# Optimization experiments

Measured on AMD Instinct MI355X. Metric: run time of the kernel, lower is better.

The kernel has to match this reference:

```python
import jax, jax.numpy as jnp
import numpy as np

EPS = 1e-12  # F.normalize eps

def _l2_normalize(x):
    n = jnp.linalg.norm(x, axis=-1, keepdims=True)
    return x / jnp.maximum(n, EPS)

def setup_inputs() -> dict:
    key = jax.random.key(0)
    k1, k2 = jax.random.split(key)
    B, C, F = 32768, 1000, 256
    features = jax.random.normal(k1, (B, F), dtype=jnp.float32)
    prototypes = jax.random.normal(k2, (C, F), dtype=jnp.float32)
    distance_scale = jnp.ones((1,), dtype=jnp.float32)
    temperature = jnp.ones((1,), dtype=jnp.float32)
    return {"features": features, "prototypes": prototypes,
            "distance_scale": distance_scale, "temperature": temperature}

def reference(features, prototypes, distance_scale, temperature):
    # Normalize both sides to the unit sphere (F.normalize, p=2, eps=1e-12)
    fn = _l2_normalize(features)       # [B, F]
    pn = _l2_normalize(prototypes)     # [C, F]
    # For unit vectors: ||a-b||_2 / sqrt(2) = sqrt(1 - a.b)
    cos = jnp.einsum('bf,cf->bc', fn, pn)          # [B, C]
    dist = jnp.sqrt(jnp.maximum(1.0 - cos, 0.0))   # cdist(...)/sqrt(2)
    iso = jnp.abs(distance_scale[0]) * dist
    logits = -(iso + jnp.mean(iso, axis=1, keepdims=True))
    return logits / temperature[0]
```

## Files before the change

### kernel.cpp

```cpp
#include <hip/hip_runtime.h>


typedef __attribute__((ext_vector_type(8))) short short8;
typedef __attribute__((ext_vector_type(4))) float f32x4;
typedef __fp16 h2 __attribute__((ext_vector_type(2)));

union U16 { uint4 u4; short8 s8; };

static __device__ __forceinline__ unsigned short f2bf(float x){
  union { float f; unsigned u; } v; v.f = x;
  unsigned r = v.u + 0x7fffu + ((v.u >> 16) & 1u);
  return (unsigned short)(r >> 16);
}

#define CPAD 1024

__global__ void norm_protos_kernel(const float* __restrict__ src,
                                   unsigned short* __restrict__ dst, int C)
{
  const int wave = threadIdx.x >> 6;
  const int lane = threadIdx.x & 63;
  const int row  = blockIdx.x * 4 + wave;
  const int t    = row >> 4;
  const int l16  = row & 15;
  const int s    = lane >> 3;
  const int quad = (lane >> 1) & 3;
  const int j    = (lane & 1) * 4;

  ushort4 o = {0, 0, 0, 0};
  if (row < C){
    const float4 v = *(const float4*)(src + row * 256 + lane * 4);
    float ss = v.x*v.x + v.y*v.y + v.z*v.z + v.w*v.w;
    #pragma unroll
    for (int off = 32; off; off >>= 1) ss += __shfl_xor(ss, off);
    const float inv = 1.0f / fmaxf(sqrtf(ss), 1e-12f);
    o.x = f2bf(v.x * inv); o.y = f2bf(v.y * inv);
    o.z = f2bf(v.z * inv); o.w = f2bf(v.w * inv);
  }
  *(ushort4*)(dst + ((size_t)((t*8 + s)*64 + quad*16 + l16))*8 + j) = o;
}

__global__ __launch_bounds__(256, 2)
void fused_kernel(const float* __restrict__ feats,
                  const unsigned short* __restrict__ pnw,
                  const float* __restrict__ ds,
                  const float* __restrict__ temp,
                  float* __restrict__ out, int C)
{
  __shared__ float wsum[2][16][4];

  const int tid  = threadIdx.x;
  const int wave = tid >> 6;
  const int lane = tid & 63;
  const int quad = lane >> 4;
  const int l16  = lane & 15;
  const long rowbase = (long)blockIdx.x * 32;

  short8 ffrag[2][8];
  #pragma unroll
  for (int rg = 0; rg < 2; ++rg){
    const float* rp = feats + (rowbase + rg*16 + l16) * 256 + quad*8;
    float4 va[8], vb[8];
    float ss = 0.f;
    #pragma unroll
    for (int s = 0; s < 8; ++s){
      va[s] = *(const float4*)(rp + s*32);
      vb[s] = *(const float4*)(rp + s*32 + 4);
      ss += va[s].x*va[s].x + va[s].y*va[s].y + va[s].z*va[s].z + va[s].w*va[s].w;
      ss += vb[s].x*vb[s].x + vb[s].y*vb[s].y + vb[s].z*vb[s].z + vb[s].w*vb[s].w;
    }
    ss += __shfl_xor(ss, 16);
    ss += __shfl_xor(ss, 32);
    const float inv = __builtin_amdgcn_rcpf(__builtin_amdgcn_sqrtf(fmaxf(ss, 1e-24f)));
    #pragma unroll
    for (int s = 0; s < 8; ++s){
      U16 u;
      u.u4.x = (unsigned)f2bf(va[s].x*inv) | ((unsigned)f2bf(va[s].y*inv) << 16);
      u.u4.y = (unsigned)f2bf(va[s].z*inv) | ((unsigned)f2bf(va[s].w*inv) << 16);
      u.u4.z = (unsigned)f2bf(vb[s].x*inv) | ((unsigned)f2bf(vb[s].y*inv) << 16);
      u.u4.w = (unsigned)f2bf(vb[s].z*inv) | ((unsigned)f2bf(vb[s].w*inv) << 16);
      ffrag[rg][s] = u.s8;
    }
  }

  const uint4* tp = (const uint4*)pnw + (size_t)(wave*16)*512 + lane;

  h2 dd0[16][2];
  h2 dd1[16][2];
  float rsum0 = 0.f, rsum1 = 0.f;

  #pragma unroll
  for (int wt = 0; wt < 16; ++wt){
    const uint4* bp = tp + (size_t)wt*512;
    short8 pfrag[8];
    #pragma unroll
    for (int s = 0; s < 8; ++s){ U16 u; u.u4 = bp[s*64]; pfrag[s] = u.s8; }

    f32x4 acc0 = (f32x4){0.f, 0.f, 0.f, 0.f};
    f32x4 acc1 = (f32x4){0.f, 0.f, 0.f, 0.f};
    #pragma unroll
    for (int s = 0; s < 8; ++s){
      acc0 = __builtin_amdgcn_mfma_f32_16x16x32_bf16(pfrag[s], ffrag[0][s], acc0, 0, 0, 0);
      acc1 = __builtin_amdgcn_mfma_f32_16x16x32_bf16(pfrag[s], ffrag[1][s], acc1, 0, 0, 0);
    }

    float a0 = __builtin_amdgcn_sqrtf(fmaxf(1.0f - acc0[0], 0.0f));
    float a1 = __builtin_amdgcn_sqrtf(fmaxf(1.0f - acc0[1], 0.0f));
    float a2 = __builtin_amdgcn_sqrtf(fmaxf(1.0f - acc0[2], 0.0f));
    float a3 = __builtin_amdgcn_sqrtf(fmaxf(1.0f - acc0[3], 0.0f));
    float b0 = __builtin_amdgcn_sqrtf(fmaxf(1.0f - acc1[0], 0.0f));
    float b1 = __builtin_amdgcn_sqrtf(fmaxf(1.0f - acc1[1], 0.0f));
    float b2 = __builtin_amdgcn_sqrtf(fmaxf(1.0f - acc1[2], 0.0f));
    float b3 = __builtin_amdgcn_sqrtf(fmaxf(1.0f - acc1[3], 0.0f));

    const int cls = wave*256 + wt*16 + quad*4;
    rsum0 += (cls < C) ? (a0 + a1 + a2 + a3) : 0.0f;
    rsum1 += (cls < C) ? (b0 + b1 + b2 + b3) : 0.0f;

    dd0[wt][0] = __builtin_amdgcn_cvt_pkrtz(a0, a1);
    dd0[wt][1] = __builtin_amdgcn_cvt_pkrtz(a2, a3);
    dd1[wt][0] = __builtin_amdgcn_cvt_pkrtz(b0, b1);
    dd1[wt][1] = __builtin_amdgcn_cvt_pkrtz(b2, b3);
  }

  rsum0 += __shfl_xor(rsum0, 16);
  rsum0 += __shfl_xor(rsum0, 32);
  rsum1 += __shfl_xor(rsum1, 16);
  rsum1 += __shfl_xor(rsum1, 32);
  if (quad == 0){
    wsum[0][l16][wave] = rsum0;
    wsum[1][l16][wave] = rsum1;
  }
  __syncthreads();

  const float nscale = -fabsf(ds[0]) / temp[0];
  const float4 w0 = *(const float4*)&wsum[0][l16][0];
  const float4 w1 = *(const float4*)&wsum[1][l16][0];
  const float bias0 = nscale * ((w0.x + w0.y + w0.z + w0.w) / (float)C);
  const float bias1 = nscale * ((w1.x + w1.y + w1.z + w1.w) / (float)C);

  float* orow0 = out + (rowbase + l16) * (size_t)C;
  float* orow1 = out + (rowbase + 16 + l16) * (size_t)C;
  #pragma unroll
  for (int wt = 0; wt < 16; ++wt){
    const int cls = wave*256 + wt*16 + quad*4;
    if (cls < C){
      float4 o0, o1;
      o0.x = fmaf(nscale, (float)dd0[wt][0][0], bias0);
      o0.y = fmaf(nscale, (float)dd0[wt][0][1], bias0);
      o0.z = fmaf(nscale, (float)dd0[wt][1][0], bias0);
      o0.w = fmaf(nscale, (float)dd0[wt][1][1], bias0);
      o1.x = fmaf(nscale, (float)dd1[wt][0][0], bias1);
      o1.y = fmaf(nscale, (float)dd1[wt][0][1], bias1);
      o1.z = fmaf(nscale, (float)dd1[wt][1][0], bias1);
      o1.w = fmaf(nscale, (float)dd1[wt][1][1], bias1);
      *(float4*)(orow0 + cls) = o0;
      *(float4*)(orow1 + cls) = o1;
    }
  }
}

extern "C" void kernel_launch(void* const* d_in, const int* in_sizes, int n_in,
                              void* d_out, int out_size, void* d_ws, size_t ws_size,
                              hipStream_t stream) {
  const float* features = (const float*)d_in[0];
  const float* protos   = (const float*)d_in[1];
  const float* dscale   = (const float*)d_in[2];
  const float* temp     = (const float*)d_in[3];
  float* out = (float*)d_out;

  const int F = 256;
  const int B = in_sizes[0] / F;
  const int C = in_sizes[1] / F;

  unsigned short* pnw = (unsigned short*)d_ws;

  norm_protos_kernel<<<CPAD/4, 256, 0, stream>>>(protos, pnw, C);
  fused_kernel<<<B/32, 256, 0, stream>>>(features, pnw, dscale, temp, out, C);
}
```

Baseline: 189.3 us.

## Prefetch prototype tiles two ahead and stage distances in LDS

Prototype fragments are loaded into a triple-buffered register ring, two tiles ahead of the MFMA loop, so global load latency overlaps with compute. Packed fp16 distances now go to a 64KB shared-memory buffer instead of 64 registers, which frees VGPRs for the prefetch buffers. The MFMA section is wrapped in s_setprio to favour matrix issue. The cost is 64KB of LDS per block, which may limit occupancy below the launch_bounds target of 2 blocks, plus extra LDS write and read traffic.

Result: faster. 185.2 us (-2.1%).

```diff
diff --git a/kernel.cpp b/kernel.cpp
--- a/kernel.cpp
+++ b/kernel.cpp
@@ -6,6 +6,7 @@
 typedef __fp16 h2 __attribute__((ext_vector_type(2)));
 
 union U16 { uint4 u4; short8 s8; };
+union H2U { h2 h; unsigned u; };
 
 static __device__ __forceinline__ unsigned short f2bf(float x){
   union { float f; unsigned u; } v; v.f = x;
@@ -47,6 +48,7 @@
                   const float* __restrict__ temp,
                   float* __restrict__ out, int C)
 {
+  __shared__ uint4 ddbuf[4 * 16 * 64];
   __shared__ float wsum[2][16][4];
 
   const int tid  = threadIdx.x;
@@ -85,24 +87,31 @@
 
   const uint4* tp = (const uint4*)pnw + (size_t)(wave*16)*512 + lane;
 
-  h2 dd0[16][2];
-  h2 dd1[16][2];
+  U16 buf[3][8];
+  #pragma unroll
+  for (int s = 0; s < 8; ++s) buf[0][s].u4 = tp[s*64];
+  #pragma unroll
+  for (int s = 0; s < 8; ++s) buf[1][s].u4 = tp[512 + s*64];
+
   float rsum0 = 0.f, rsum1 = 0.f;
 
   #pragma unroll
   for (int wt = 0; wt < 16; ++wt){
-    const uint4* bp = tp + (size_t)wt*512;
-    short8 pfrag[8];
-    #pragma unroll
-    for (int s = 0; s < 8; ++s){ U16 u; u.u4 = bp[s*64]; pfrag[s] = u.s8; }
+    if (wt + 2 < 16){
+      const uint4* np = tp + (size_t)(wt + 2)*512;
+      #pragma unroll
+      for (int s = 0; s < 8; ++s) buf[(wt + 2) % 3][s].u4 = np[s*64];
+    }
 
     f32x4 acc0 = (f32x4){0.f, 0.f, 0.f, 0.f};
     f32x4 acc1 = (f32x4){0.f, 0.f, 0.f, 0.f};
+    __builtin_amdgcn_s_setprio(1);
     #pragma unroll
     for (int s = 0; s < 8; ++s){
-      acc0 = __builtin_amdgcn_mfma_f32_16x16x32_bf16(pfrag[s], ffrag[0][s], acc0, 0, 0, 0);
-      acc1 = __builtin_amdgcn_mfma_f32_16x16x32_bf16(pfrag[s], ffrag[1][s], acc1, 0, 0, 0);
+      acc0 = __builtin_amdgcn_mfma_f32_16x16x32_bf16(buf[wt % 3][s].s8, ffrag[0][s], acc0, 0, 0, 0);
+      acc1 = __builtin_amdgcn_mfma_f32_16x16x32_bf16(buf[wt % 3][s].s8, ffrag[1][s], acc1, 0, 0, 0);
     }
+    __builtin_amdgcn_s_setprio(0);
 
     float a0 = __builtin_amdgcn_sqrtf(fmaxf(1.0f - acc0[0], 0.0f));
     float a1 = __builtin_amdgcn_sqrtf(fmaxf(1.0f - acc0[1], 0.0f));
@@ -117,10 +126,13 @@
     rsum0 += (cls < C) ? (a0 + a1 + a2 + a3) : 0.0f;
     rsum1 += (cls < C) ? (b0 + b1 + b2 + b3) : 0.0f;
 
-    dd0[wt][0] = __builtin_amdgcn_cvt_pkrtz(a0, a1);
-    dd0[wt][1] = __builtin_amdgcn_cvt_pkrtz(a2, a3);
-    dd1[wt][0] = __builtin_amdgcn_cvt_pkrtz(b0, b1);
-    dd1[wt][1] = __builtin_amdgcn_cvt_pkrtz(b2, b3);
+    H2U p0, p1, p2, p3;
+    p0.h = __builtin_amdgcn_cvt_pkrtz(a0, a1);
+    p1.h = __builtin_amdgcn_cvt_pkrtz(a2, a3);
+    p2.h = __builtin_amdgcn_cvt_pkrtz(b0, b1);
+    p3.h = __builtin_amdgcn_cvt_pkrtz(b2, b3);
+    uint4 pk; pk.x = p0.u; pk.y = p1.u; pk.z = p2.u; pk.w = p3.u;
+    ddbuf[(wave*16 + wt)*64 + lane] = pk;
   }
 
   rsum0 += __shfl_xor(rsum0, 16);
@@ -145,15 +157,18 @@
   for (int wt = 0; wt < 16; ++wt){
     const int cls = wave*256 + wt*16 + quad*4;
     if (cls < C){
+      const uint4 pk = ddbuf[(wave*16 + wt)*64 + lane];
+      H2U p0, p1, p2, p3;
+      p0.u = pk.x; p1.u = pk.y; p2.u = pk.z; p3.u = pk.w;
       float4 o0, o1;
-      o0.x = fmaf(nscale, (float)dd0[wt][0][0], bias0);
-      o0.y = fmaf(nscale, (float)dd0[wt][0][1], bias0);
-      o0.z = fmaf(nscale, (float)dd0[wt][1][0], bias0);
-      o0.w = fmaf(nscale, (float)dd0[wt][1][1], bias0);
-      o1.x = fmaf(nscale, (float)dd1[wt][0][0], bias1);
-      o1.y = fmaf(nscale, (float)dd1[wt][0][1], bias1);
-      o1.z = fmaf(nscale, (float)dd1[wt][1][0], bias1);
-      o1.w = fmaf(nscale, (float)dd1[wt][1][1], bias1);
+      o0.x = fmaf(nscale, (float)p0.h[0], bias0);
+      o0.y = fmaf(nscale, (float)p0.h[1], bias0);
+      o0.z = fmaf(nscale, (float)p1.h[0], bias0);
+      o0.w = fmaf(nscale, (float)p1.h[1], bias0);
+      o1.x = fmaf(nscale, (float)p2.h[0], bias1);
+      o1.y = fmaf(nscale, (float)p2.h[1], bias1);
+      o1.z = fmaf(nscale, (float)p3.h[0], bias1);
+      o1.w = fmaf(nscale, (float)p3.h[1], bias1);
       *(float4*)(orow0 + cls) = o0;
       *(float4*)(orow1 + cls) = o1;
     }
```

## Process two row batches per block, overlapping first batch's stores with second's MFMAs

Applied to the files above, without the earlier changes.

Each block now handles 64 rows as two 32-row batches. The first batch's packed distances are parked in LDS and written out during the second batch's MFMA loop, so output stores overlap tensor-core work. Prototype fragments are double-buffered in registers so the next tile's loads are issued before the current tile's compute. MFMA sections are also wrapped in s_setprio. The cost is 64KB of LDS per block, more register pressure, and half as many blocks, which may reduce occupancy.

Result: slower. 204.3 us (+7.9%).

```diff
diff --git a/kernel.cpp b/kernel.cpp
--- a/kernel.cpp
+++ b/kernel.cpp
@@ -6,6 +6,7 @@
 typedef __fp16 h2 __attribute__((ext_vector_type(2)));
 
 union U16 { uint4 u4; short8 s8; };
+union H2U { h2 h; unsigned u; };
 
 static __device__ __forceinline__ unsigned short f2bf(float x){
   union { float f; unsigned u; } v; v.f = x;
@@ -47,115 +48,171 @@
                   const float* __restrict__ temp,
                   float* __restrict__ out, int C)
 {
-  __shared__ float wsum[2][16][4];
+  __shared__ uint4 ddbuf[4 * 16 * 64];
+  __shared__ float wsum[2][2][16][4];
 
   const int tid  = threadIdx.x;
   const int wave = tid >> 6;
   const int lane = tid & 63;
   const int quad = lane >> 4;
   const int l16  = lane & 15;
-  const long rowbase = (long)blockIdx.x * 32;
-
-  short8 ffrag[2][8];
+  const long rowbase0 = (long)blockIdx.x * 64;
+
+  const float nscale = -fabsf(ds[0]) / temp[0];
+  const uint4* tp = (const uint4*)pnw + (size_t)(wave*16)*512 + lane;
+
+  float biasP0 = 0.f, biasP1 = 0.f;
+  float* orowP0 = nullptr;
+  float* orowP1 = nullptr;
+
   #pragma unroll
-  for (int rg = 0; rg < 2; ++rg){
-    const float* rp = feats + (rowbase + rg*16 + l16) * 256 + quad*8;
-    float4 va[8], vb[8];
-    float ss = 0.f;
-    #pragma unroll
-    for (int s = 0; s < 8; ++s){
-      va[s] = *(const float4*)(rp + s*32);
-      vb[s] = *(const float4*)(rp + s*32 + 4);
-      ss += va[s].x*va[s].x + va[s].y*va[s].y + va[s].z*va[s].z + va[s].w*va[s].w;
-      ss += vb[s].x*vb[s].x + vb[s].y*vb[s].y + vb[s].z*vb[s].z + vb[s].w*vb[s].w;
-    }
-    ss += __shfl_xor(ss, 16);
-    ss += __shfl_xor(ss, 32);
-    const float inv = __builtin_amdgcn_rcpf(__builtin_amdgcn_sqrtf(fmaxf(ss, 1e-24f)));
-    #pragma unroll
-    for (int s = 0; s < 8; ++s){
-      U16 u;
-      u.u4.x = (unsigned)f2bf(va[s].x*inv) | ((unsigned)f2bf(va[s].y*inv) << 16);
-      u.u4.y = (unsigned)f2bf(va[s].z*inv) | ((unsigned)f2bf(va[s].w*inv) << 16);
-      u.u4.z = (unsigned)f2bf(vb[s].x*inv) | ((unsigned)f2bf(vb[s].y*inv) << 16);
-      u.u4.w = (unsigned)f2bf(vb[s].z*inv) | ((unsigned)f2bf(vb[s].w*inv) << 16);
-      ffrag[rg][s] = u.s8;
-    }
-  }
-
-  const uint4* tp = (const uint4*)pnw + (size_t)(wave*16)*512 + lane;
-
-  h2 dd0[16][2];
-  h2 dd1[16][2];
-  float rsum0 = 0.f, rsum1 = 0.f;
-
-  #pragma unroll
-  for (int wt = 0; wt < 16; ++wt){
-    const uint4* bp = tp + (size_t)wt*512;
-    short8 pfrag[8];
-    #pragma unroll
-    for (int s = 0; s < 8; ++s){ U16 u; u.u4 = bp[s*64]; pfrag[s] = u.s8; }
-
-    f32x4 acc0 = (f32x4){0.f, 0.f, 0.f, 0.f};
-    f32x4 acc1 = (f32x4){0.f, 0.f, 0.f, 0.f};
-    #pragma unroll
-    for (int s = 0; s < 8; ++s){
-      acc0 = __builtin_amdgcn_mfma_f32_16x16x32_bf16(pfrag[s], ffrag[0][s], acc0, 0, 0, 0);
-      acc1 = __builtin_amdgcn_mfma_f32_16x16x32_bf16(pfrag[s], ffrag[1][s], acc1, 0, 0, 0);
-    }
-
-    float a0 = __builtin_amdgcn_sqrtf(fmaxf(1.0f - acc0[0], 0.0f));
-    float a1 = __builtin_amdgcn_sqrtf(fmaxf(1.0f - acc0[1], 0.0f));
-    float a2 = __builtin_amdgcn_sqrtf(fmaxf(1.0f - acc0[2], 0.0f));
-    float a3 = __builtin_amdgcn_sqrtf(fmaxf(1.0f - acc0[3], 0.0f));
-    float b0 = __builtin_amdgcn_sqrtf(fmaxf(1.0f - acc1[0], 0.0f));
-    float b1 = __builtin_amdgcn_sqrtf(fmaxf(1.0f - acc1[1], 0.0f));
-    float b2 = __builtin_amdgcn_sqrtf(fmaxf(1.0f - acc1[2], 0.0f));
-    float b3 = __builtin_amdgcn_sqrtf(fmaxf(1.0f - acc1[3], 0.0f));
-
-    const int cls = wave*256 + wt*16 + quad*4;
-    rsum0 += (cls < C) ? (a0 + a1 + a2 + a3) : 0.0f;
-    rsum1 += (cls < C) ? (b0 + b1 + b2 + b3) : 0.0f;
-
-    dd0[wt][0] = __builtin_amdgcn_cvt_pkrtz(a0, a1);
-    dd0[wt][1] = __builtin_amdgcn_cvt_pkrtz(a2, a3);
-    dd1[wt][0] = __builtin_amdgcn_cvt_pkrtz(b0, b1);
-    dd1[wt][1] = __builtin_amdgcn_cvt_pkrtz(b2, b3);
-  }
-
-  rsum0 += __shfl_xor(rsum0, 16);
-  rsum0 += __shfl_xor(rsum0, 32);
-  rsum1 += __shfl_xor(rsum1, 16);
-  rsum1 += __shfl_xor(rsum1, 32);
-  if (quad == 0){
-    wsum[0][l16][wave] = rsum0;
-    wsum[1][l16][wave] = rsum1;
-  }
-  __syncthreads();
-
-  const float nscale = -fabsf(ds[0]) / temp[0];
-  const float4 w0 = *(const float4*)&wsum[0][l16][0];
-  const float4 w1 = *(const float4*)&wsum[1][l16][0];
-  const float bias0 = nscale * ((w0.x + w0.y + w0.z + w0.w) / (float)C);
-  const float bias1 = nscale * ((w1.x + w1.y + w1.z + w1.w) / (float)C);
-
-  float* orow0 = out + (rowbase + l16) * (size_t)C;
-  float* orow1 = out + (rowbase + 16 + l16) * (size_t)C;
-  #pragma unroll
-  for (int wt = 0; wt < 16; ++wt){
-    const int cls = wave*256 + wt*16 + quad*4;
-    if (cls < C){
-      float4 o0, o1;
-      o0.x = fmaf(nscale, (float)dd0[wt][0][0], bias0);
-      o0.y = fmaf(nscale, (float)dd0[wt][0][1], bias0);
-      o0.z = fmaf(nscale, (float)dd0[wt][1][0], bias0);
-      o0.w = fmaf(nscale, (float)dd0[wt][1][1], bias0);
-      o1.x = fmaf(nscale, (float)dd1[wt][0][0], bias1);
-      o1.y = fmaf(nscale, (float)dd1[wt][0][1], bias1);
-      o1.z = fmaf(nscale, (float)dd1[wt][1][0], bias1);
-      o1.w = fmaf(nscale, (float)dd1[wt][1][1], bias1);
-      *(float4*)(orow0 + cls) = o0;
-      *(float4*)(orow1 + cls) = o1;
+  for (int b = 0; b < 2; ++b){
+    const long rb = rowbase0 + b*32;
+
+    short8 ffrag[2][8];
+    #pragma unroll
+    for (int rg = 0; rg < 2; ++rg){
+      const float* rp = feats + (rb + rg*16 + l16) * 256 + quad*8;
+      float4 va[8], vb[8];
+      float ss = 0.f;
+      #pragma unroll
+      for (int s = 0; s < 8; ++s){
+        va[s] = *(const float4*)(rp + s*32);
+        vb[s] = *(const float4*)(rp + s*32 + 4);
+        ss += va[s].x*va[s].x + va[s].y*va[s].y + va[s].z*va[s].z + va[s].w*va[s].w;
+        ss += vb[s].x*vb[s].x + vb[s].y*vb[s].y + vb[s].z*vb[s].z + vb[s].w*vb[s].w;
+      }
+      ss += __shfl_xor(ss, 16);
+      ss += __shfl_xor(ss, 32);
+      const float inv = __builtin_amdgcn_rcpf(__builtin_amdgcn_sqrtf(fmaxf(ss, 1e-24f)));
+      #pragma unroll
+      for (int s = 0; s < 8; ++s){
+        U16 u;
+        u.u4.x = (unsigned)f2bf(va[s].x*inv) | ((unsigned)f2bf(va[s].y*inv) << 16);
+        u.u4.y = (unsigned)f2bf(va[s].z*inv) | ((unsigned)f2bf(va[s].w*inv) << 16);
+        u.u4.z = (unsigned)f2bf(vb[s].x*inv) | ((unsigned)f2bf(vb[s].y*inv) << 16);
+        u.u4.w = (unsigned)f2bf(vb[s].z*inv) | ((unsigned)f2bf(vb[s].w*inv) << 16);
+        ffrag[rg][s] = u.s8;
+      }
+    }
+
+    U16 bufA[8], bufB[8];
+    #pragma unroll
+    for (int s = 0; s < 8; ++s) bufA[s].u4 = tp[s*64];
+
+    h2 dd0[16][2];
+    h2 dd1[16][2];
+    float rsum0 = 0.f, rsum1 = 0.f;
+
+    #pragma unroll
+    for (int wt = 0; wt < 16; ++wt){
+      if (wt + 1 < 16){
+        const uint4* np = tp + (size_t)(wt + 1)*512;
+        if ((wt & 1) == 0){
+          #pragma unroll
+          for (int s = 0; s < 8; ++s) bufB[s].u4 = np[s*64];
+        } else {
+          #pragma unroll
+          for (int s = 0; s < 8; ++s) bufA[s].u4 = np[s*64];
+        }
+      }
+
+      f32x4 acc0 = (f32x4){0.f, 0.f, 0.f, 0.f};
+      f32x4 acc1 = (f32x4){0.f, 0.f, 0.f, 0.f};
+      __builtin_amdgcn_s_setprio(1);
+      #pragma unroll
+      for (int s = 0; s < 8; ++s){
+        const short8 pf = ((wt & 1) == 0) ? bufA[s].s8 : bufB[s].s8;
+        acc0 = __builtin_amdgcn_mfma_f32_16x16x32_bf16(pf, ffrag[0][s], acc0, 0, 0, 0);
+        acc1 = __builtin_amdgcn_mfma_f32_16x16x32_bf16(pf, ffrag[1][s], acc1, 0, 0, 0);
+      }
+      __builtin_amdgcn_s_setprio(0);
+
+      float a0 = __builtin_amdgcn_sqrtf(fmaxf(1.0f - acc0[0], 0.0f));
+      float a1 = __builtin_amdgcn_sqrtf(fmaxf(1.0f - acc0[1], 0.0f));
+      float a2 = __builtin_amdgcn_sqrtf(fmaxf(1.0f - acc0[2], 0.0f));
+      float a3 = __builtin_amdgcn_sqrtf(fmaxf(1.0f - acc0[3], 0.0f));
+      float b0 = __builtin_amdgcn_sqrtf(fmaxf(1.0f - acc1[0], 0.0f));
+      float b1 = __builtin_amdgcn_sqrtf(fmaxf(1.0f - acc1[1], 0.0f));
+      float b2 = __builtin_amdgcn_sqrtf(fmaxf(1.0f - acc1[2], 0.0f));
+      float b3 = __builtin_amdgcn_sqrtf(fmaxf(1.0f - acc1[3], 0.0f));
+
+      const int cls = wave*256 + wt*16 + quad*4;
+      rsum0 += (cls < C) ? (a0 + a1 + a2 + a3) : 0.0f;
+      rsum1 += (cls < C) ? (b0 + b1 + b2 + b3) : 0.0f;
+
+      dd0[wt][0] = __builtin_amdgcn_cvt_pkrtz(a0, a1);
+      dd0[wt][1] = __builtin_amdgcn_cvt_pkrtz(a2, a3);
+      dd1[wt][0] = __builtin_amdgcn_cvt_pkrtz(b0, b1);
+      dd1[wt][1] = __builtin_amdgcn_cvt_pkrtz(b2, b3);
+
+      if (b == 1){
+        const uint4 pk = ddbuf[(wave*16 + wt)*64 + lane];
+        if (cls < C){
+          H2U p0, p1, p2, p3;
+          p0.u = pk.x; p1.u = pk.y; p2.u = pk.z; p3.u = pk.w;
+          float4 o0, o1;
+          o0.x = fmaf(nscale, (float)p0.h[0], biasP0);
+          o0.y = fmaf(nscale, (float)p0.h[1], biasP0);
+          o0.z = fmaf(nscale, (float)p1.h[0], biasP0);
+          o0.w = fmaf(nscale, (float)p1.h[1], biasP0);
+          o1.x = fmaf(nscale, (float)p2.h[0], biasP1);
+          o1.y = fmaf(nscale, (float)p2.h[1], biasP1);
+          o1.z = fmaf(nscale, (float)p3.h[0], biasP1);
+          o1.w = fmaf(nscale, (float)p3.h[1], biasP1);
+          *(float4*)(orowP0 + cls) = o0;
+          *(float4*)(orowP1 + cls) = o1;
+        }
+      }
+    }
+
+    rsum0 += __shfl_xor(rsum0, 16);
+    rsum0 += __shfl_xor(rsum0, 32);
+    rsum1 += __shfl_xor(rsum1, 16);
+    rsum1 += __shfl_xor(rsum1, 32);
+    if (quad == 0){
+      wsum[b][0][l16][wave] = rsum0;
+      wsum[b][1][l16][wave] = rsum1;
+    }
+    __syncthreads();
+
+    const float4 w0 = *(const float4*)&wsum[b][0][l16][0];
+    const float4 w1 = *(const float4*)&wsum[b][1][l16][0];
+    const float bias0 = nscale * ((w0.x + w0.y + w0.z + w0.w) / (float)C);
+    const float bias1 = nscale * ((w1.x + w1.y + w1.z + w1.w) / (float)C);
+
+    if (b == 0){
+      #pragma unroll
+      for (int wt = 0; wt < 16; ++wt){
+        H2U p0, p1, p2, p3;
+        p0.h = dd0[wt][0]; p1.h = dd0[wt][1];
+        p2.h = dd1[wt][0]; p3.h = dd1[wt][1];
+        uint4 pk; pk.x = p0.u; pk.y = p1.u; pk.z = p2.u; pk.w = p3.u;
+        ddbuf[(wave*16 + wt)*64 + lane] = pk;
+      }
+      biasP0 = bias0; biasP1 = bias1;
+      orowP0 = out + (rb + l16) * (size_t)C;
+      orowP1 = out + (rb + 16 + l16) * (size_t)C;
+    } else {
+      float* orow0 = out + (rb + l16) * (size_t)C;
+      float* orow1 = out + (rb + 16 + l16) * (size_t)C;
+      #pragma unroll
+      for (int wt = 0; wt < 16; ++wt){
+        const int cls = wave*256 + wt*16 + quad*4;
+        if (cls < C){
+          float4 o0, o1;
+          o0.x = fmaf(nscale, (float)dd0[wt][0][0], bias0);
+          o0.y = fmaf(nscale, (float)dd0[wt][0][1], bias0);
+          o0.z = fmaf(nscale, (float)dd0[wt][1][0], bias0);
+          o0.w = fmaf(nscale, (float)dd0[wt][1][1], bias0);
+          o1.x = fmaf(nscale, (float)dd1[wt][0][0], bias1);
+          o1.y = fmaf(nscale, (float)dd1[wt][0][1], bias1);
+          o1.z = fmaf(nscale, (float)dd1[wt][1][0], bias1);
+          o1.w = fmaf(nscale, (float)dd1[wt][1][1], bias1);
+          *(float4*)(orow0 + cls) = o0;
+          *(float4*)(orow1 + cls) = o1;
+        }
+      }
     }
   }
 }
@@ -176,5 +233,5 @@
   unsigned short* pnw = (unsigned short*)d_ws;
 
   norm_protos_kernel<<<CPAD/4, 256, 0, stream>>>(protos, pnw, C);
-  fused_kernel<<<B/32, 256, 0, stream>>>(features, pnw, dscale, temp, out, C);
-}
+  fused_kernel<<<B/64, 256, 0, stream>>>(features, pnw, dscale, temp, out, C);
+}
```

## Halve rows per block to raise occupancy, add MFMA priority and nontemporal stores

Applied to the files above, without the earlier changes.

Each block now handles 16 feature rows instead of 32, which halves the per-thread register footprint (fragments and packed distance buffers). Launch bounds move from 2 to 4 blocks per SIMD to raise occupancy and hide the latency of the 131 MB output write. It also raises wave priority around the MFMA chain and writes the output with nontemporal stores to avoid polluting cache. The trade-off is that each prototype fragment loaded from memory now feeds half as many MFMAs, doubling prototype traffic through L2.

New measurement: 227.7 us. 20.3% more time.

```diff
diff --git a/kernel.cpp b/kernel.cpp
--- a/kernel.cpp
+++ b/kernel.cpp
@@ -40,26 +40,25 @@
   *(ushort4*)(dst + ((size_t)((t*8 + s)*64 + quad*16 + l16))*8 + j) = o;
 }
 
-__global__ __launch_bounds__(256, 2)
+__global__ __launch_bounds__(256, 4)
 void fused_kernel(const float* __restrict__ feats,
                   const unsigned short* __restrict__ pnw,
                   const float* __restrict__ ds,
                   const float* __restrict__ temp,
                   float* __restrict__ out, int C)
 {
-  __shared__ float wsum[2][16][4];
+  __shared__ float wsum[16][4];
 
   const int tid  = threadIdx.x;
   const int wave = tid >> 6;
   const int lane = tid & 63;
   const int quad = lane >> 4;
   const int l16  = lane & 15;
-  const long rowbase = (long)blockIdx.x * 32;
+  const long rowbase = (long)blockIdx.x * 16;
 
-  short8 ffrag[2][8];
-  #pragma unroll
-  for (int rg = 0; rg < 2; ++rg){
-    const float* rp = feats + (rowbase + rg*16 + l16) * 256 + quad*8;
+  short8 ffrag[8];
+  {
+    const float* rp = feats + (rowbase + l16) * 256 + quad*8;
     float4 va[8], vb[8];
     float ss = 0.f;
     #pragma unroll
@@ -79,15 +78,14 @@
       u.u4.y = (unsigned)f2bf(va[s].z*inv) | ((unsigned)f2bf(va[s].w*inv) << 16);
       u.u4.z = (unsigned)f2bf(vb[s].x*inv) | ((unsigned)f2bf(vb[s].y*inv) << 16);
       u.u4.w = (unsigned)f2bf(vb[s].z*inv) | ((unsigned)f2bf(vb[s].w*inv) << 16);
-      ffrag[rg][s] = u.s8;
+      ffrag[s] = u.s8;
     }
   }
 
   const uint4* tp = (const uint4*)pnw + (size_t)(wave*16)*512 + lane;
 
-  h2 dd0[16][2];
-  h2 dd1[16][2];
-  float rsum0 = 0.f, rsum1 = 0.f;
+  h2 dd[16][2];
+  float rsum = 0.f;
 
   #pragma unroll
   for (int wt = 0; wt < 16; ++wt){
@@ -96,66 +94,46 @@
     #pragma unroll
     for (int s = 0; s < 8; ++s){ U16 u; u.u4 = bp[s*64]; pfrag[s] = u.s8; }
 
-    f32x4 acc0 = (f32x4){0.f, 0.f, 0.f, 0.f};
-    f32x4 acc1 = (f32x4){0.f, 0.f, 0.f, 0.f};
+    f32x4 acc = (f32x4){0.f, 0.f, 0.f, 0.f};
+    __builtin_amdgcn_s_setprio(1);
     #pragma unroll
-    for (int s = 0; s < 8; ++s){
-      acc0 = __builtin_amdgcn_mfma_f32_16x16x32_bf16(pfrag[s], ffrag[0][s], acc0, 0, 0, 0);
-      acc1 = __builtin_amdgcn_mfma_f32_16x16x32_bf16(pfrag[s], ffrag[1][s], acc1, 0, 0, 0);
-    }
+    for (int s = 0; s < 8; ++s)
+      acc = __builtin_amdgcn_mfma_f32_16x16x32_bf16(pfrag[s], ffrag[s], acc, 0, 0, 0);
+    __builtin_amdgcn_s_setprio(0);
 
-    float a0 = __builtin_amdgcn_sqrtf(fmaxf(1.0f - acc0[0], 0.0f));
-    float a1 = __builtin_amdgcn_sqrtf(fmaxf(1.0f - acc0[1], 0.0f));
-    float a2 = __builtin_amdgcn_sqrtf(fmaxf(1.0f - acc0[2], 0.0f));
-    float a3 = __builtin_amdgcn_sqrtf(fmaxf(1.0f - acc0[3], 0.0f));
-    float b0 = __builtin_amdgcn_sqrtf(fmaxf(1.0f - acc1[0], 0.0f));
-    float b1 = __builtin_amdgcn_sqrtf(fmaxf(1.0f - acc1[1], 0.0f));
-    float b2 = __builtin_amdgcn_sqrtf(fmaxf(1.0f - acc1[2], 0.0f));
-    float b3 = __builtin_amdgcn_sqrtf(fmaxf(1.0f - acc1[3], 0.0f));
+    float d0 = __builtin_amdgcn_sqrtf(fmaxf(1.0f - acc[0], 0.0f));
+    float d1 = __builtin_amdgcn_sqrtf(fmaxf(1.0f - acc[1], 0.0f));
+    float d2 = __builtin_amdgcn_sqrtf(fmaxf(1.0f - acc[2], 0.0f));
+    float d3 = __builtin_amdgcn_sqrtf(fmaxf(1.0f - acc[3], 0.0f));
 
     const int cls = wave*256 + wt*16 + quad*4;
-    rsum0 += (cls < C) ? (a0 + a1 + a2 + a3) : 0.0f;
-    rsum1 += (cls < C) ? (b0 + b1 + b2 + b3) : 0.0f;
+    rsum += (cls < C) ? (d0 + d1 + d2 + d3) : 0.0f;
 
-    dd0[wt][0] = __builtin_amdgcn_cvt_pkrtz(a0, a1);
-    dd0[wt][1] = __builtin_amdgcn_cvt_pkrtz(a2, a3);
-    dd1[wt][0] = __builtin_amdgcn_cvt_pkrtz(b0, b1);
-    dd1[wt][1] = __builtin_amdgcn_cvt_pkrtz(b2, b3);
+    dd[wt][0] = __builtin_amdgcn_cvt_pkrtz(d0, d1);
+    dd[wt][1] = __builtin_amdgcn_cvt_pkrtz(d2, d3);
   }
 
-  rsum0 += __shfl_xor(rsum0, 16);
-  rsum0 += __shfl_xor(rsum0, 32);
-  rsum1 += __shfl_xor(rsum1, 16);
-  rsum1 += __shfl_xor(rsum1, 32);
-  if (quad == 0){
-    wsum[0][l16][wave] = rsum0;
-    wsum[1][l16][wave] = rsum1;
-  }
+  rsum += __shfl_xor(rsum, 16);
+  rsum += __shfl_xor(rsum, 32);
+  if (quad == 0) wsum[l16][wave] = rsum;
   __syncthreads();
 
+  const float4 wv = *(const float4*)&wsum[l16][0];
+  const float mean = (wv.x + wv.y + wv.z + wv.w) / (float)C;
   const float nscale = -fabsf(ds[0]) / temp[0];
-  const float4 w0 = *(const float4*)&wsum[0][l16][0];
-  const float4 w1 = *(const float4*)&wsum[1][l16][0];
-  const float bias0 = nscale * ((w0.x + w0.y + w0.z + w0.w) / (float)C);
-  const float bias1 = nscale * ((w1.x + w1.y + w1.z + w1.w) / (float)C);
+  const float bias = nscale * mean;
 
-  float* orow0 = out + (rowbase + l16) * (size_t)C;
-  float* orow1 = out + (rowbase + 16 + l16) * (size_t)C;
+  float* orow = out + (rowbase + l16) * (size_t)C;
   #pragma unroll
   for (int wt = 0; wt < 16; ++wt){
     const int cls = wave*256 + wt*16 + quad*4;
     if (cls < C){
-      float4 o0, o1;
-      o0.x = fmaf(nscale, (float)dd0[wt][0][0], bias0);
-      o0.y = fmaf(nscale, (float)dd0[wt][0][1], bias0);
-      o0.z = fmaf(nscale, (float)dd0[wt][1][0], bias0);
-      o0.w = fmaf(nscale, (float)dd0[wt][1][1], bias0);
-      o1.x = fmaf(nscale, (float)dd1[wt][0][0], bias1);
-      o1.y = fmaf(nscale, (float)dd1[wt][0][1], bias1);
-      o1.z = fmaf(nscale, (float)dd1[wt][1][0], bias1);
-      o1.w = fmaf(nscale, (float)dd1[wt][1][1], bias1);
-      *(float4*)(orow0 + cls) = o0;
-      *(float4*)(orow1 + cls) = o1;
+      f32x4 o;
+      o[0] = fmaf(nscale, (float)dd[wt][0][0], bias);
+      o[1] = fmaf(nscale, (float)dd[wt][0][1], bias);
+      o[2] = fmaf(nscale, (float)dd[wt][1][0], bias);
+      o[3] = fmaf(nscale, (float)dd[wt][1][1], bias);
+      __builtin_nontemporal_store(o, (f32x4*)(orow + cls));
     }
   }
 }
@@ -176,5 +154,5 @@
   unsigned short* pnw = (unsigned short*)d_ws;
 
   norm_protos_kernel<<<CPAD/4, 256, 0, stream>>>(protos, pnw, C);
-  fused_kernel<<<B/32, 256, 0, stream>>>(features, pnw, dscale, temp, out, C);
+  fused_kernel<<<B/16, 256, 0, stream>>>(features, pnw, dscale, temp, out, C);
 }
```
